# Performance work log

Measured on AMD Instinct MI355X. Metric: run time of the kernel, lower is better.

## Reference

```python
import jax, jax.numpy as jnp
import numpy as np

B, H, W = 4, 768, 768
K = 4096            # max zero-crossing points kept per sample (padded/masked)
UPDATE_SCALE = 1.0
DIST_THRESHOLD = 3.0
W_INJECT = 1.0
W_PIXEL = 1.0
EPS = 1e-8
BIG = 1e30          # stand-in for +inf distance of invalid gt points


def _make_sdf(radius, center, key):
    # signed distance to a circle + smooth low-frequency perturbation -> realistic SDF
    r = jnp.arange(H, dtype=jnp.float32)[:, None]
    c = jnp.arange(W, dtype=jnp.float32)[None, :]
    d = jnp.sqrt((r - center[0]) ** 2 + (c - center[1]) ** 2) - radius
    noise = jax.random.normal(key, (H // 32, W // 32), dtype=jnp.float32)
    noise = jax.image.resize(noise, (H, W), method='bilinear') * 2.0
    return d + noise


def setup_inputs() -> dict:
    key = jax.random.key(0)
    ks = jax.random.split(key, 2 * B)
    preds, gts = [], []
    for b in range(B):
        cr, cc = H / 2 + 10 * b, W / 2 - 7 * b
        preds.append(_make_sdf(240.0 + 3 * b, (cr, cc), ks[2 * b]))
        gts.append(_make_sdf(250.0 - 2 * b, (cr + 5, cc - 4), ks[2 * b + 1]))
    return {"pred_sdf": jnp.stack(preds), "gt_sdf": jnp.stack(gts)}


def extract_zc(sdf):
    """Padded zero-crossing extraction: returns (K,2) coords and (K,) valid mask."""
    v1, v2 = sdf[:-1, :], sdf[1:, :]
    mask_v = (v1 * v2) < 0
    alpha_v = jnp.abs(v1) / (jnp.abs(v1) + jnp.abs(v2) + EPS)
    rs_v = jnp.arange(H - 1, dtype=jnp.float32)[:, None] + alpha_v          # (H-1,W)
    cs_v = jnp.broadcast_to(jnp.arange(W, dtype=jnp.float32)[None, :], (H - 1, W))

    h1, h2 = sdf[:, :-1], sdf[:, 1:]
    mask_h = (h1 * h2) < 0
    alpha_h = jnp.abs(h1) / (jnp.abs(h1) + jnp.abs(h2) + EPS)
    rs_h = jnp.broadcast_to(jnp.arange(H, dtype=jnp.float32)[:, None], (H, W - 1))
    cs_h = jnp.arange(W - 1, dtype=jnp.float32)[None, :] + alpha_h          # (H,W-1)

    mask_z = sdf == 0
    rz = jnp.broadcast_to(jnp.arange(H, dtype=jnp.float32)[:, None], (H, W))
    cz = jnp.broadcast_to(jnp.arange(W, dtype=jnp.float32)[None, :], (H, W))

    pts = jnp.concatenate([
        jnp.stack([rz.ravel(), cz.ravel()], -1),
        jnp.stack([rs_v.ravel(), cs_v.ravel()], -1),
        jnp.stack([rs_h.ravel(), cs_h.ravel()], -1)], axis=0)               # (M,2)
    mask = jnp.concatenate([mask_z.ravel(), mask_v.ravel(), mask_h.ravel()])
    order = jnp.argsort(~mask)[:K]      # stable sort -> True (crossing) entries first
    return pts[order], mask[order]


def compute_normals(sdf):
    gr = jnp.zeros_like(sdf)
    gr = gr.at[1:-1].set(0.5 * (sdf[2:] - sdf[:-2]))
    gr = gr.at[0].set(sdf[1] - sdf[0]).at[-1].set(sdf[-1] - sdf[-2])
    gc = jnp.zeros_like(sdf)
    gc = gc.at[:, 1:-1].set(0.5 * (sdf[:, 2:] - sdf[:, :-2]))
    gc = gc.at[:, 0].set(sdf[:, 1] - sdf[:, 0]).at[:, -1].set(sdf[:, -1] - sdf[:, -2])
    return jnp.stack([gr, gc], -1)      # (H,W,2)


def _corner(coords):
    r, c = coords[:, 0], coords[:, 1]
    r0 = jnp.clip(jnp.floor(r).astype(jnp.int32), 0, H - 1)
    c0 = jnp.clip(jnp.floor(c).astype(jnp.int32), 0, W - 1)
    r1 = jnp.clip(r0 + 1, 0, H - 1)
    c1 = jnp.clip(c0 + 1, 0, W - 1)
    ar = r - r0.astype(jnp.float32)
    ac = c - c0.astype(jnp.float32)
    return r0, c0, r1, c1, ar, ac


def bilinear_sample(img, coords):
    r0, c0, r1, c1, ar, ac = _corner(coords)
    return (img[r0, c0] * (1 - ar) * (1 - ac) + img[r0, c1] * (1 - ar) * ac
            + img[r1, c0] * ar * (1 - ac) + img[r1, c1] * ar * ac)


def chamfer_grad(pred2d, pred_zc, valid_p, gt_zc, valid_g):
    normals = compute_normals(pred2d)
    r0, c0, r1, c1, ar, ac = _corner(pred_zc)
    n = (normals[r0, c0] * ((1 - ar) * (1 - ac))[:, None]
         + normals[r0, c1] * ((1 - ar) * ac)[:, None]
         + normals[r1, c0] * (ar * (1 - ac))[:, None]
         + normals[r1, c1] * (ar * ac)[:, None])
    n = n / (jnp.linalg.norm(n, axis=1, keepdims=True) + 1e-8)

    diff = gt_zc[None, :, :] - pred_zc[:, None, :]          # (Kp,Kg,2)
    dist = jnp.linalg.norm(diff, axis=-1)                   # (Kp,Kg)
    dist = jnp.where(valid_g[None, :], dist, BIG)
    idx = jnp.argmin(dist, axis=1)
    min_dist = jnp.take_along_axis(dist, idx[:, None], 1)[:, 0]
    mask = (min_dist <= DIST_THRESHOLD) & valid_p & jnp.any(valid_g)
    dir_vec = jnp.take_along_axis(diff, idx[:, None, None], 1)[:, 0, :]
    dot = (dir_vec * n).sum(1) * UPDATE_SCALE
    dot = jnp.where(mask, dot, 0.0)

    w00 = (1 - ar) * (1 - ac); w01 = (1 - ar) * ac
    w10 = ar * (1 - ac);       w11 = ar * ac
    flat = lambda rr, cc: rr * W + cc
    indices = jnp.concatenate([flat(r0, c0), flat(r0, c1), flat(r1, c0), flat(r1, c1)])
    contribs = jnp.concatenate([dot * w00, dot * w01, dot * w10, dot * w11])
    dflat = jnp.zeros(H * W, dtype=pred2d.dtype).at[indices].add(contribs)
    return dflat.reshape(H, W)


def _per_sample(pred2d, gt2d):
    gt_zc, valid_g = extract_zc(gt2d)
    # torch uses pred.detach() for zero-crossing locations
    pred_zc, valid_p = extract_zc(jax.lax.stop_gradient(pred2d))
    dSDF = chamfer_grad(pred2d, pred_zc, valid_p, gt_zc, valid_g)
    inject = jnp.sum(pred2d * jax.lax.stop_gradient(dSDF))
    pixel = jnp.sum(jnp.where(valid_p, bilinear_sample(pred2d, pred_zc), 0.0))
    return inject, pixel


def reference(pred_sdf, gt_sdf):
    inject, pixel = jax.vmap(_per_sample)(pred_sdf, gt_sdf)
    return W_INJECT * inject.mean() + W_PIXEL * pixel.mean()
```

## Files before the change

### kernel.cpp

```cpp
#include <hip/hip_runtime.h>
#include <climits>


typedef unsigned long long ull;

constexpr int B = 4, H = 768, W = 768, K = 4096;
constexpr int HW = H * W;
constexpr int NFIELD = 2 * B;
constexpr int BANDS = 256;
constexpr int WPR = W / 64;
constexpr int SEGW = 768 * WPR;
constexpr int MSTRIDE = 3 * SEGW;
constexpr int GSPLIT = 16;
constexpr int GRNG = K / GSPLIT;
constexpr int IBLK = K / 256;
constexpr int NDBLK = B * HW / 256;

constexpr size_t alignup(size_t x, size_t a) { return (x + a - 1) & ~(a - 1); }

constexpr size_t OFF_ACC   = 0;
constexpr size_t OFF_CNT   = OFF_ACC + sizeof(double) * 8;
constexpr size_t OFF_WCNT  = OFF_CNT + sizeof(int) * NFIELD;
constexpr size_t OFF_MASKS = alignup(OFF_WCNT + sizeof(int) * NFIELD * 768, 8);
constexpr size_t OFF_PTS   = OFF_MASKS + sizeof(ull) * NFIELD * MSTRIDE;
constexpr size_t OFF_NNKEY = OFF_PTS + sizeof(float2) * NFIELD * K;
constexpr size_t OFF_HEADS = alignup(OFF_NNKEY + sizeof(ull) * (size_t)B * K, 16);
constexpr size_t OFF_NXT   = OFF_HEADS + sizeof(int) * (size_t)B * HW;
constexpr size_t OFF_EVAL  = OFF_NXT + sizeof(int) * (size_t)B * 4 * K;
constexpr size_t OFF_DIRTY = OFF_EVAL + sizeof(float) * (size_t)B * 4 * K;
constexpr size_t WS_NEED   = OFF_DIRTY + sizeof(int) * NDBLK;

#define DEVFN __device__ __forceinline__

DEVFN float grad_r(const float* __restrict__ s, int r, int c) {
#pragma clang fp contract(off)
  if (r == 0)      return s[W + c] - s[c];
  if (r == H - 1)  return s[(H - 1) * W + c] - s[(H - 2) * W + c];
  return 0.5f * (s[(r + 1) * W + c] - s[(r - 1) * W + c]);
}
DEVFN float grad_c(const float* __restrict__ s, int r, int c) {
#pragma clang fp contract(off)
  if (c == 0)      return s[r * W + 1] - s[r * W];
  if (c == W - 1)  return s[r * W + W - 1] - s[r * W + W - 2];
  return 0.5f * (s[r * W + c + 1] - s[r * W + c - 1]);
}

DEVFN const float* field_sdf(const float* pred, const float* gt, int f) {
  return ((f & 1) ? gt : pred) + (size_t)(f >> 1) * HW;
}

__global__ __launch_bounds__(256) void k_count(const float* __restrict__ pred,
                                               const float* __restrict__ gt,
                                               ull* __restrict__ masks,
                                               int* __restrict__ wave_cnt,
                                               int* __restrict__ heads,
                                               int* __restrict__ dirty,
                                               ull* __restrict__ nnkey,
                                               double* __restrict__ acc) {
#pragma clang fp contract(off)
  int gtid = blockIdx.x * 256 + (int)threadIdx.x;
  int gsz = gridDim.x * 256;
  int4* h4 = (int4*)heads;
  for (int idx = gtid; idx < B * HW / 4; idx += gsz)
    h4[idx] = make_int4(-1, -1, -1, -1);
  for (int idx = gtid; idx < NDBLK; idx += gsz) dirty[idx] = 0;
  for (int idx = gtid; idx < B * K; idx += gsz) nnkey[idx] = ~0ull;
  if (gtid < 8) acc[gtid] = 0.0;

  int f = blockIdx.x >> 6;
  int bb = blockIdx.x & 63;
  int wave = threadIdx.x >> 6, lane = threadIdx.x & 63;
  int band = bb * 4 + wave;
  int r0 = band * 3;
  const float* sdf = field_sdf(pred, gt, f);
  ull* mz = masks + (size_t)f * MSTRIDE;
  ull* mv = mz + SEGW;
  ull* mh = mv + SEGW;

  float cur[WPR], nxt[WPR];
#pragma unroll
  for (int i = 0; i < WPR; ++i) cur[i] = sdf[r0 * W + i * 64 + lane];
  int cz = 0, cv = 0, ch = 0;
  for (int rr = 0; rr < 3; ++rr) {
    int row = r0 + rr;
    bool hasNext = row < H - 1;
    if (hasNext) {
#pragma unroll
      for (int i = 0; i < WPR; ++i) nxt[i] = sdf[(row + 1) * W + i * 64 + lane];
    }
#pragma unroll
    for (int i = 0; i < WPR; ++i) {
      ull m = __ballot(cur[i] == 0.0f);
      if (lane == 0) mz[row * WPR + i] = m;
      cz += __popcll(m);
      float nb = __shfl_down(cur[i], 1);
      float nb2 = (i < WPR - 1) ? __shfl(cur[i + 1], 0) : 0.0f;
      if (lane == 63) nb = nb2;
      bool hp = (i * 64 + lane < W - 1) && (cur[i] * nb < 0.0f);
      m = __ballot(hp);
      if (lane == 0) mh[row * WPR + i] = m;
      ch += __popcll(m);
      if (hasNext) {
        m = __ballot(cur[i] * nxt[i] < 0.0f);
        if (lane == 0) mv[row * WPR + i] = m;
        cv += __popcll(m);
      }
    }
    if (hasNext) {
#pragma unroll
      for (int i = 0; i < WPR; ++i) cur[i] = nxt[i];
    }
  }
  if (lane == 0) {
    int* wc = wave_cnt + f * 768;
    wc[0 * BANDS + band] = cz;
    wc[1 * BANDS + band] = cv;
    wc[2 * BANDS + band] = ch;
  }
}

__global__ __launch_bounds__(256) void k_emit(const float* __restrict__ pred,
                                              const float* __restrict__ gt,
                                              const ull* __restrict__ masks,
                                              const int* __restrict__ wave_cnt,
                                              float2* __restrict__ pts,
                                              int* __restrict__ counts_raw) {
#pragma clang fp contract(off)
  int f = blockIdx.x / 192;
  int tb = blockIdx.x - f * 192;
  __shared__ int cnt_s[768];
  for (int t = threadIdx.x; t < 768; t += 256) cnt_s[t] = wave_cnt[f * 768 + t];
  __syncthreads();
  int wave = threadIdx.x >> 6, lane = threadIdx.x & 63;
  int task = tb * 4 + wave;
  int seg = task >> 8, band = task & 255;
  int a = 0;
  for (int idx = lane; idx < task; idx += 64) a += cnt_s[idx];
  for (int off = 32; off > 0; off >>= 1) a += __shfl_xor(a, off, 64);
  int base = a;
  if (tb == 0 && wave == 0) {
    int t2 = 0;
    for (int idx = lane; idx < 768; idx += 64) t2 += cnt_s[idx];
    for (int off = 32; off > 0; off >>= 1) t2 += __shfl_xor(t2, off, 64);
    if (lane == 0) counts_raw[f] = t2;
  }
  if (base >= K) return;
  const float* sdf = field_sdf(pred, gt, f);
  const ull* mseg = masks + (size_t)f * MSTRIDE + (size_t)seg * SEGW;
  float2* fp = pts + (size_t)f * K;
  int r0 = band * 3;
  for (int rr = 0; rr < 3; ++rr) {
    int row = r0 + rr;
    if (seg == 1 && row >= H - 1) break;
    for (int i = 0; i < WPR; ++i) {
      ull m = mseg[row * WPR + i];
      if (!m) continue;
      if ((m >> lane) & 1ull) {
        int c = i * 64 + lane;
        float pr, pc;
        if (seg == 0) {
          pr = (float)row; pc = (float)c;
        } else if (seg == 1) {
          float v1 = sdf[row * W + c], v2 = sdf[(row + 1) * W + c];
          float a1 = fabsf(v1), a2 = fabsf(v2);
          float alpha = a1 / ((a1 + a2) + 1e-8f);
          pr = (float)row + alpha; pc = (float)c;
        } else {
          float h1 = sdf[row * W + c], h2 = sdf[row * W + c + 1];
          float a1 = fabsf(h1), a2 = fabsf(h2);
          float alpha = a1 / ((a1 + a2) + 1e-8f);
          pr = (float)row; pc = (float)c + alpha;
        }
        int pos = base + __popcll(m & ((1ull << lane) - 1ull));
        if (pos < K) fp[pos] = make_float2(pr, pc);
      }
      base += __popcll(m);
      if (base >= K) { rr = 3; break; }
    }
  }
}

__global__ __launch_bounds__(256) void k_nn(const float2* __restrict__ pts,
                                            const int* __restrict__ counts_raw,
                                            ull* __restrict__ nnkey) {
#pragma clang fp contract(off)
  int b = blockIdx.x >> 8;
  int rem = blockIdx.x & 255;
  int ib = rem >> 4, ig = rem & 15;
  int tid = (int)threadIdx.x;
  int np_ = min(counts_raw[2 * b + 0], K);
  int ng  = min(counts_raw[2 * b + 1], K);
  int j0 = ig * GRNG;
  int n = min(GRNG, ng - j0);
  const float2* gp = pts + (size_t)(2 * b + 1) * K;

  __shared__ float2 tile[GRNG];
  __shared__ float smin[256], smax[256];
  float rmin = __builtin_inff(), rmax = -__builtin_inff();
  if (tid < n) {
    float2 g = gp[j0 + tid];
    tile[tid] = g;
    rmin = g.x; rmax = g.x;
  }
  smin[tid] = rmin; smax[tid] = rmax;
  __syncthreads();
  for (int s = 128; s > 0; s >>= 1) {
    if (tid < s) {
      smin[tid] = fminf(smin[tid], smin[tid + s]);
      smax[tid] = fmaxf(smax[tid], smax[tid + s]);
    }
    __syncthreads();
  }
  float gmin = smin[0] - 3.001f, gmax = smax[0] + 3.001f;

  int i = ib * 256 + tid;
  if (i >= np_ || n <= 0) return;
  float2 q = pts[(size_t)(2 * b) * K + i];
  float pr = q.x, pc = q.y;
  if (pr < gmin || pr > gmax) return;
  float best = __builtin_inff();
  unsigned bj = 0xffffffffu;
#pragma unroll 4
  for (int j = 0; j < n; ++j) {
    float dr = tile[j].x - pr;
    float dc = tile[j].y - pc;
    float sqf = fmaf(dr, dr, dc * dc);
    if (sqf <= 9.0001f) {
      float d = sqrtf((dr * dr) + (dc * dc));
      if (d < best) { best = d; bj = (unsigned)(j0 + j); }
    }
  }
  if (bj != 0xffffffffu)
    atomicMin(&nnkey[(size_t)b * K + i],
              ((ull)__float_as_uint(best) << 32) | bj);
}

__global__ __launch_bounds__(256) void k_post(const float* __restrict__ pred,
                                              const float2* __restrict__ pts,
                                              const int* __restrict__ counts_raw,
                                              const ull* __restrict__ nnkey,
                                              int* __restrict__ heads,
                                              int* __restrict__ nxt,
                                              float* __restrict__ eval,
                                              int* __restrict__ dirty,
                                              double* __restrict__ acc) {
#pragma clang fp contract(off)
  int b = blockIdx.x >> 4;
  int i = ((blockIdx.x & 15) << 8) + (int)threadIdx.x;
  const float* P = pred + (size_t)b * HW;
  int np_ = min(counts_raw[2 * b + 0], K);
  bool active = (i < np_);
  float sval = 0.0f;
  if (active) {
    ull key = nnkey[(size_t)b * K + i];
    float2 q = pts[(size_t)(2 * b) * K + i];
    float pr = q.x, pc = q.y;

    int r0 = (int)floorf(pr); r0 = r0 < 0 ? 0 : (r0 > H - 1 ? H - 1 : r0);
    int c0 = (int)floorf(pc); c0 = c0 < 0 ? 0 : (c0 > W - 1 ? W - 1 : c0);
    int r1 = (r0 + 1 > H - 1) ? H - 1 : r0 + 1;
    int c1 = (c0 + 1 > W - 1) ? W - 1 : c0 + 1;
    float ar = pr - (float)r0;
    float ac = pc - (float)c0;
    float omr = 1.0f - ar, omc = 1.0f - ac;
    float u00 = omr * omc, u01 = omr * ac, u10 = ar * omc, u11 = ar * ac;

    float v00 = P[r0 * W + c0], v01 = P[r0 * W + c1];
    float v10 = P[r1 * W + c0], v11 = P[r1 * W + c1];
    sval = (v00 * omr) * omc + (v01 * omr) * ac + (v10 * ar) * omc + (v11 * ar) * ac;

    float best = __uint_as_float((unsigned)(key >> 32));
    if (best <= 3.0f) {
      const float2* gp = pts + (size_t)(2 * b + 1) * K;
      float2 g = gp[(unsigned)(key & 0xffffffffu)];
      float grA = grad_r(P, r0, c0), grB = grad_r(P, r0, c1);
      float grC = grad_r(P, r1, c0), grD = grad_r(P, r1, c1);
      float gcA = grad_c(P, r0, c0), gcB = grad_c(P, r0, c1);
      float gcC = grad_c(P, r1, c0), gcD = grad_c(P, r1, c1);
      float n_r = ((grA * u00 + grB * u01) + grC * u10) + grD * u11;
      float n_c = ((gcA * u00 + gcB * u01) + gcC * u10) + gcD * u11;
      float nn = sqrtf((n_r * n_r) + (n_c * n_c));
      float den = nn + 1e-8f;
      float nrm_r = n_r / den, nrm_c = n_c / den;
      float dr = g.x - pr, dc = g.y - pc;
      float dot = (dr * nrm_r) + (dc * nrm_c);
      dot = dot * 1.0f;
      if (dot != 0.0f) {
        int px[4] = { r0 * W + c0, r0 * W + c1, r1 * W + c0, r1 * W + c1 };
        float cv[4] = { dot * u00, dot * u01, dot * u10, dot * u11 };
        int basee = b * 4 * K;
        for (int k2 = 0; k2 < 4; ++k2) {
          int e = k2 * K + i;
          eval[basee + e] = cv[k2];
          nxt[basee + e] = atomicExch(&heads[(size_t)b * HW + px[k2]], e);
          dirty[(b * HW + px[k2]) >> 8] = 1;
        }
      }
    }
  }
  __shared__ double red[256];
  red[threadIdx.x] = (double)sval;
  __syncthreads();
  for (int s = 128; s > 0; s >>= 1) {
    if ((int)threadIdx.x < s) red[threadIdx.x] += red[threadIdx.x + s];
    __syncthreads();
  }
  if (threadIdx.x == 0 && red[0] != 0.0) atomicAdd(&acc[4 + b], red[0]);
}

__global__ __launch_bounds__(256) void k_gather(const float* __restrict__ pred,
                                                const int* __restrict__ heads,
                                                const int* __restrict__ nxt,
                                                const float* __restrict__ eval,
                                                const int* __restrict__ dirty,
                                                double* __restrict__ acc) {
#pragma clang fp contract(off)
  if (!dirty[blockIdx.x]) return;
  int idx = blockIdx.x * 256 + (int)threadIdx.x;
  int b = idx / HW;
  float term = 0.0f;
  int h = heads[idx];
  if (h >= 0) {
    int base = b * 4 * K;
    float facc = 0.0f;
    int last = -1;
    for (;;) {
      int bestE = INT_MAX;
      for (int e = h; e >= 0; e = nxt[base + e])
        if (e > last && e < bestE) bestE = e;
      if (bestE == INT_MAX) break;
      facc = facc + eval[base + bestE];
      last = bestE;
    }
    term = pred[idx] * facc;
  }
  __shared__ double red[256];
  red[threadIdx.x] = (double)term;
  __syncthreads();
  for (int s = 128; s > 0; s >>= 1) {
    if ((int)threadIdx.x < s) red[threadIdx.x] += red[threadIdx.x + s];
    __syncthreads();
  }
  if (threadIdx.x == 0 && red[0] != 0.0)
    atomicAdd(&acc[blockIdx.x * 256 / HW], red[0]);
}

__global__ void k_final(const double* __restrict__ acc, float* __restrict__ out) {
  if (threadIdx.x == 0 && blockIdx.x == 0) {
    double mi = (acc[0] + acc[1] + acc[2] + acc[3]) * 0.25;
    double mp = (acc[4] + acc[5] + acc[6] + acc[7]) * 0.25;
    out[0] = (float)(mi + mp);
  }
}

extern "C" void kernel_launch(void* const* d_in, const int* in_sizes, int n_in,
                              void* d_out, int out_size, void* d_ws, size_t ws_size,
                              hipStream_t stream) {
  const float* pred = (const float*)d_in[0];
  const float* gt   = (const float*)d_in[1];
  float* out = (float*)d_out;
  char* ws = (char*)d_ws;

  double* acc        = (double*)(ws + OFF_ACC);
  int*    counts_raw = (int*)(ws + OFF_CNT);
  int*    wave_cnt   = (int*)(ws + OFF_WCNT);
  ull*    masks      = (ull*)(ws + OFF_MASKS);
  float2* pts        = (float2*)(ws + OFF_PTS);
  ull*    nnkey      = (ull*)(ws + OFF_NNKEY);
  int*    heads      = (int*)(ws + OFF_HEADS);
  int*    nxt        = (int*)(ws + OFF_NXT);
  float*  eval       = (float*)(ws + OFF_EVAL);
  int*    dirty      = (int*)(ws + OFF_DIRTY);

  (void)in_sizes; (void)n_in; (void)out_size; (void)ws_size;

  k_count<<<dim3(NFIELD * 64), dim3(256), 0, stream>>>(pred, gt, masks, wave_cnt,
                                                       heads, dirty, nnkey, acc);
  k_emit<<<dim3(NFIELD * 192), dim3(256), 0, stream>>>(pred, gt, masks, wave_cnt,
                                                       pts, counts_raw);
  k_nn<<<dim3(B * IBLK * GSPLIT), dim3(256), 0, stream>>>(pts, counts_raw, nnkey);
  k_post<<<dim3(B * IBLK), dim3(256), 0, stream>>>(pred, pts, counts_raw, nnkey,
                                                   heads, nxt, eval, dirty, acc);
  k_gather<<<dim3(NDBLK), dim3(256), 0, stream>>>(pred, heads, nxt, eval, dirty, acc);
  k_final<<<dim3(1), dim3(1), 0, stream>>>(acc, out);
}
```

Before: 90.31 us.

## Fuse gather and final reduction with last-block-done counters and bucketed accumulators

```diff
diff --git a/kernel.cpp b/kernel.cpp
--- a/kernel.cpp
+++ b/kernel.cpp
@@ -15,12 +15,18 @@
 constexpr int GRNG = K / GSPLIT;
 constexpr int IBLK = K / 256;
 constexpr int NDBLK = B * HW / 256;
+constexpr int NGB = 1024;
+constexpr int TPG = NDBLK / NGB;
+constexpr int NBKT = 16;
 
 constexpr size_t alignup(size_t x, size_t a) { return (x + a - 1) & ~(a - 1); }
 
 constexpr size_t OFF_ACC   = 0;
-constexpr size_t OFF_CNT   = OFF_ACC + sizeof(double) * 8;
-constexpr size_t OFF_WCNT  = OFF_CNT + sizeof(int) * NFIELD;
+constexpr size_t OFF_BACC  = OFF_ACC + sizeof(double) * 8;
+constexpr size_t OFF_CNT   = OFF_BACC + sizeof(double) * NBKT * 8;
+constexpr size_t OFF_MESO  = OFF_CNT + sizeof(int) * NFIELD;
+constexpr size_t OFF_MST   = OFF_MESO + sizeof(int) * 16 * 32;
+constexpr size_t OFF_WCNT  = OFF_MST + sizeof(int) * 4;
 constexpr size_t OFF_MASKS = alignup(OFF_WCNT + sizeof(int) * NFIELD * 768, 8);
 constexpr size_t OFF_PTS   = OFF_MASKS + sizeof(ull) * NFIELD * MSTRIDE;
 constexpr size_t OFF_NNKEY = OFF_PTS + sizeof(float2) * NFIELD * K;
@@ -56,6 +62,9 @@
                                                int* __restrict__ heads,
                                                int* __restrict__ dirty,
                                                ull* __restrict__ nnkey,
+                                               double* __restrict__ bacc,
+                                               int* __restrict__ meso,
+                                               int* __restrict__ master,
                                                double* __restrict__ acc) {
 #pragma clang fp contract(off)
   int gtid = blockIdx.x * 256 + (int)threadIdx.x;
@@ -66,6 +75,9 @@
   for (int idx = gtid; idx < NDBLK; idx += gsz) dirty[idx] = 0;
   for (int idx = gtid; idx < B * K; idx += gsz) nnkey[idx] = ~0ull;
   if (gtid < 8) acc[gtid] = 0.0;
+  if (gtid >= 64 && gtid < 64 + NBKT * 8) bacc[gtid - 64] = 0.0;
+  if (gtid >= 256 && gtid < 256 + 16 * 32) meso[gtid - 256] = 0;
+  if (gtid == 1024) *master = 0;
 
   int f = blockIdx.x >> 6;
   int bb = blockIdx.x & 63;
@@ -308,48 +320,66 @@
   if (threadIdx.x == 0 && red[0] != 0.0) atomicAdd(&acc[4 + b], red[0]);
 }
 
-__global__ __launch_bounds__(256) void k_gather(const float* __restrict__ pred,
-                                                const int* __restrict__ heads,
-                                                const int* __restrict__ nxt,
-                                                const float* __restrict__ eval,
-                                                const int* __restrict__ dirty,
-                                                double* __restrict__ acc) {
-#pragma clang fp contract(off)
-  if (!dirty[blockIdx.x]) return;
-  int idx = blockIdx.x * 256 + (int)threadIdx.x;
-  int b = idx / HW;
-  float term = 0.0f;
-  int h = heads[idx];
-  if (h >= 0) {
-    int base = b * 4 * K;
-    float facc = 0.0f;
-    int last = -1;
-    for (;;) {
-      int bestE = INT_MAX;
-      for (int e = h; e >= 0; e = nxt[base + e])
-        if (e > last && e < bestE) bestE = e;
-      if (bestE == INT_MAX) break;
-      facc = facc + eval[base + bestE];
-      last = bestE;
-    }
-    term = pred[idx] * facc;
-  }
+__global__ __launch_bounds__(256) void k_gather_final(const float* __restrict__ pred,
+                                                      const int* __restrict__ heads,
+                                                      const int* __restrict__ nxt,
+                                                      const float* __restrict__ eval,
+                                                      const int* __restrict__ dirty,
+                                                      double* __restrict__ bacc,
+                                                      int* __restrict__ meso,
+                                                      int* __restrict__ master,
+                                                      double* __restrict__ acc,
+                                                      float* __restrict__ out) {
+#pragma clang fp contract(off)
+  int tid = (int)threadIdx.x;
   __shared__ double red[256];
-  red[threadIdx.x] = (double)term;
-  __syncthreads();
-  for (int s = 128; s > 0; s >>= 1) {
-    if ((int)threadIdx.x < s) red[threadIdx.x] += red[threadIdx.x + s];
+  for (int t = 0; t < TPG; ++t) {
+    int tile = blockIdx.x + t * NGB;
+    if (!dirty[tile]) continue;
+    int idx = tile * 256 + tid;
+    int b = idx / HW;
+    float term = 0.0f;
+    int h = heads[idx];
+    if (h >= 0) {
+      int base = b * 4 * K;
+      float facc = 0.0f;
+      int last = -1;
+      for (;;) {
+        int bestE = INT_MAX;
+        for (int e = h; e >= 0; e = nxt[base + e])
+          if (e > last && e < bestE) bestE = e;
+        if (bestE == INT_MAX) break;
+        facc = facc + eval[base + bestE];
+        last = bestE;
+      }
+      term = pred[idx] * facc;
+    }
+    red[tid] = (double)term;
     __syncthreads();
-  }
-  if (threadIdx.x == 0 && red[0] != 0.0)
-    atomicAdd(&acc[blockIdx.x * 256 / HW], red[0]);
-}
-
-__global__ void k_final(const double* __restrict__ acc, float* __restrict__ out) {
-  if (threadIdx.x == 0 && blockIdx.x == 0) {
-    double mi = (acc[0] + acc[1] + acc[2] + acc[3]) * 0.25;
-    double mp = (acc[4] + acc[5] + acc[6] + acc[7]) * 0.25;
-    out[0] = (float)(mi + mp);
+    for (int s = 128; s > 0; s >>= 1) {
+      if (tid < s) red[tid] += red[tid + s];
+      __syncthreads();
+    }
+    if (tid == 0 && red[0] != 0.0)
+      atomicAdd(&bacc[(blockIdx.x & (NBKT - 1)) * 8 + b], red[0]);
+    __syncthreads();
+  }
+  if (tid == 0) {
+    __threadfence();
+    int old = atomicAdd(&meso[(blockIdx.x >> 6) * 32], 1);
+    if (old == 63) {
+      int o2 = atomicAdd(master, 1);
+      if (o2 == 15) {
+        __threadfence();
+        double mi = 0.0, mp = 0.0;
+        for (int k2 = 0; k2 < NBKT; ++k2)
+          for (int b2 = 0; b2 < B; ++b2)
+            mi += atomicAdd(&bacc[k2 * 8 + b2], 0.0);
+        for (int b2 = 0; b2 < B; ++b2)
+          mp += atomicAdd(&acc[4 + b2], 0.0);
+        out[0] = (float)(mi * 0.25 + mp * 0.25);
+      }
+    }
   }
 }
 
@@ -362,7 +392,10 @@
   char* ws = (char*)d_ws;
 
   double* acc        = (double*)(ws + OFF_ACC);
+  double* bacc       = (double*)(ws + OFF_BACC);
   int*    counts_raw = (int*)(ws + OFF_CNT);
+  int*    meso       = (int*)(ws + OFF_MESO);
+  int*    master     = (int*)(ws + OFF_MST);
   int*    wave_cnt   = (int*)(ws + OFF_WCNT);
   ull*    masks      = (ull*)(ws + OFF_MASKS);
   float2* pts        = (float2*)(ws + OFF_PTS);
@@ -375,12 +408,13 @@
   (void)in_sizes; (void)n_in; (void)out_size; (void)ws_size;
 
   k_count<<<dim3(NFIELD * 64), dim3(256), 0, stream>>>(pred, gt, masks, wave_cnt,
-                                                       heads, dirty, nnkey, acc);
+                                                       heads, dirty, nnkey,
+                                                       bacc, meso, master, acc);
   k_emit<<<dim3(NFIELD * 192), dim3(256), 0, stream>>>(pred, gt, masks, wave_cnt,
                                                        pts, counts_raw);
   k_nn<<<dim3(B * IBLK * GSPLIT), dim3(256), 0, stream>>>(pts, counts_raw, nnkey);
   k_post<<<dim3(B * IBLK), dim3(256), 0, stream>>>(pred, pts, counts_raw, nnkey,
                                                    heads, nxt, eval, dirty, acc);
-  k_gather<<<dim3(NDBLK), dim3(256), 0, stream>>>(pred, heads, nxt, eval, dirty, acc);
-  k_final<<<dim3(1), dim3(1), 0, stream>>>(acc, out);
-}
+  k_gather_final<<<dim3(NGB), dim3(256), 0, stream>>>(pred, heads, nxt, eval, dirty,
+                                                      bacc, meso, master, acc, out);
+}
```

Result: slower. 118.9 us (+31.7%).
